# Optimization experiments

Hardware: AMD Instinct MI355X
Metric: run time of the kernel (lower is better)

The kernel has to match this reference:

```python
import jax, jax.numpy as jnp
import numpy as np

B, N, D, H = 8, 1024, 512, 8
DH = D // H  # one_head_dim = 64


def setup_inputs() -> dict:
    key = jax.random.key(0)
    ks = jax.random.split(key, 7)
    s = 0.02
    return {
        "x": jax.random.normal(ks[0], (B, N, D), dtype=jnp.float32),
        "bias": jax.random.normal(ks[1], (B, N, N, H), dtype=jnp.float32),
        "Wq": jax.random.normal(ks[2], (D, D), dtype=jnp.float32) * s,
        "Wk": jax.random.normal(ks[3], (D, D), dtype=jnp.float32) * s,
        "Wv": jax.random.normal(ks[4], (D, D), dtype=jnp.float32) * s,
        "Wm": jax.random.normal(ks[5], (D, D), dtype=jnp.float32) * s,
        "bm": jnp.zeros((D,), dtype=jnp.float32),
    }


def reference(x, bias, Wq, Wk, Wv, Wm, bm):
    # Linear layers (torch Linear: y = x @ W.T); dropout is identity at eval.
    scale = DH ** -0.5
    q = (x @ Wq.T).reshape(B, N, H, DH).transpose(0, 2, 1, 3) * scale  # [B,H,N,DH]
    k = (x @ Wk.T).reshape(B, N, H, DH).transpose(0, 2, 1, 3)
    v = (x @ Wv.T).reshape(B, N, H, DH).transpose(0, 2, 1, 3)
    # scores + additive pairwise bias (bias permuted [B,N,N,H] -> [B,H,N,N])
    scores = jnp.einsum("bhnd,bhmd->bhnm", q, k) + bias.transpose(0, 3, 1, 2)
    attn = jax.nn.softmax(scores, axis=-1)
    out = jnp.einsum("bhnm,bhmd->bhnd", attn, v)  # [B,H,N,DH]
    out = out.transpose(0, 2, 1, 3).reshape(B, N, D)
    return out @ Wm.T + bm
```

## Files before the change

kernel.cpp:

```cpp
#include <hip/hip_runtime.h>
#include <hip/hip_bf16.h>

typedef __bf16 bf16x8 __attribute__((ext_vector_type(8)));
typedef __bf16 bf16x4 __attribute__((ext_vector_type(4)));
typedef float  f32x4  __attribute__((ext_vector_type(4)));

#define MFMA16(a, b, c) __builtin_amdgcn_mfma_f32_16x16x32_bf16((a), (b), (c), 0, 0, 0)

typedef const __attribute__((address_space(1))) unsigned int* gas_t;
typedef __attribute__((address_space(3))) unsigned int* las_t;
__device__ __forceinline__ void dma16(const __bf16* g, __bf16* l) {
    __builtin_amdgcn_global_load_lds((gas_t)g, (las_t)l, 16, 0, 0);
}


__global__ __launch_bounds__(256) void gemm_qkv(
    const float* __restrict__ x,
    const float* __restrict__ Wq, const float* __restrict__ Wk,
    const float* __restrict__ Wv,
    __bf16* __restrict__ qo, __bf16* __restrict__ ko, __bf16* __restrict__ vto)
{
    __shared__ __bf16 As[64][40];
    __shared__ __bf16 Bs[3][64][40];
    const int tid  = threadIdx.x;
    const int lane = tid & 63;
    const int wid  = tid >> 6;
    const int g    = lane >> 4, l16 = lane & 15;
    const int wr   = wid >> 1,  wc  = wid & 1;
    const int r0   = blockIdx.x * 64;
    const int c0   = blockIdx.y * 64;
    const float* Ws[3] = { Wq, Wk, Wv };

    const int sr  = tid >> 3;
    const int scq = tid & 7;

    f32x4 acc[3][2][2] = {};

    for (int k0 = 0; k0 < 512; k0 += 32) {
        __syncthreads();
#pragma unroll
        for (int j = 0; j < 2; ++j) {
            const int r = sr + 32 * j;
            float4 av = *reinterpret_cast<const float4*>(x + (size_t)(r0 + r) * 512 + k0 + scq * 4);
            bf16x4 ap = { (__bf16)av.x, (__bf16)av.y, (__bf16)av.z, (__bf16)av.w };
            *reinterpret_cast<bf16x4*>(&As[r][scq * 4]) = ap;
#pragma unroll
            for (int widx = 0; widx < 3; ++widx) {
                float4 bv = *reinterpret_cast<const float4*>(Ws[widx] + (size_t)(c0 + r) * 512 + k0 + scq * 4);
                bf16x4 bp = { (__bf16)bv.x, (__bf16)bv.y, (__bf16)bv.z, (__bf16)bv.w };
                *reinterpret_cast<bf16x4*>(&Bs[widx][r][scq * 4]) = bp;
            }
        }
        __syncthreads();
        bf16x8 af[2];
#pragma unroll
        for (int rt = 0; rt < 2; ++rt)
            af[rt] = *reinterpret_cast<const bf16x8*>(&As[wr * 32 + rt * 16 + l16][g * 8]);
#pragma unroll
        for (int widx = 0; widx < 3; ++widx) {
            bf16x8 bfr[2];
#pragma unroll
            for (int ct = 0; ct < 2; ++ct)
                bfr[ct] = *reinterpret_cast<const bf16x8*>(&Bs[widx][wc * 32 + ct * 16 + l16][g * 8]);
#pragma unroll
            for (int rt = 0; rt < 2; ++rt)
#pragma unroll
                for (int ct = 0; ct < 2; ++ct)
                    acc[widx][rt][ct] = MFMA16(af[rt], bfr[ct], acc[widx][rt][ct]);
        }
    }

#pragma unroll
    for (int widx = 0; widx < 2; ++widx) {
        __bf16* dst = (widx == 0) ? qo : ko;
        const float scale = (widx == 0) ? 0.125f : 1.0f;
#pragma unroll
        for (int rt = 0; rt < 2; ++rt)
#pragma unroll
            for (int ct = 0; ct < 2; ++ct)
#pragma unroll
                for (int reg = 0; reg < 4; ++reg) {
                    int r = r0 + wr * 32 + rt * 16 + 4 * g + reg;
                    int c = c0 + wc * 32 + ct * 16 + l16;
                    float val = acc[widx][rt][ct][reg] * scale;
                    int b = r >> 10, n = r & 1023, h = c >> 6, dh = c & 63;
                    dst[(((size_t)b * 8 + h) * 1024 + n) * 64 + dh] = (__bf16)val;
                }
    }
#pragma unroll
    for (int rt = 0; rt < 2; ++rt)
#pragma unroll
        for (int ct = 0; ct < 2; ++ct) {
            int r = r0 + wr * 32 + rt * 16 + 4 * g;
            int c = c0 + wc * 32 + ct * 16 + l16;
            int b = r >> 10, n = r & 1023, h = c >> 6, dh = c & 63;
            bf16x4 pv = { (__bf16)acc[2][rt][ct][0], (__bf16)acc[2][rt][ct][1],
                          (__bf16)acc[2][rt][ct][2], (__bf16)acc[2][rt][ct][3] };
            size_t addr = (((size_t)(b * 8 + h) * 32 + (n >> 5)) * 64 + dh) * 32 + (n & 31);
            *reinterpret_cast<bf16x4*>(vto + addr) = pv;
        }
}

__global__ __launch_bounds__(512, 2) void attn_v12(
    const __bf16* __restrict__ qw, const __bf16* __restrict__ kw,
    const __bf16* __restrict__ vtw, const float* __restrict__ bias,
    __bf16* __restrict__ ow)
{
    __shared__ __align__(16) __bf16 Ks[8][32][64];
    __shared__ __align__(16) __bf16 Vs[8][64][32];
    __shared__ __align__(16) __bf16 bsm[2][8][32][36];
    __shared__ __bf16 psm[8][32][40];
    const int tid  = threadIdx.x;
    const int w    = tid >> 6;
    const int lane = tid & 63;
    const int g    = lane >> 4, l16 = lane & 15;
    const int b    = blockIdx.x;
    const int n0   = blockIdx.y * 32;
    const size_t bhs = (size_t)b * 8 + w;

    const __bf16* kbase  = kw  + bhs * 1024 * 64;
    const __bf16* vbase  = vtw + bhs * 32 * 2048;
    const float*  bias_b = bias + ((size_t)(b * 1024 + n0)) * 8192;

    const int snr = tid >> 4;
    const int sf  = tid & 15;

    const int k_row  = lane >> 3;
    const int k_csrc = (lane & 7) ^ (k_row & 7);
    const int v_dh   = lane >> 2;
    const int v_csrc = (lane & 3) ^ ((lane >> 3) & 3);
    const int v_rsw  = (l16 >> 1) & 3;

    bf16x8 qf[2][2];
#pragma unroll
    for (int rf = 0; rf < 2; ++rf)
#pragma unroll
        for (int kc = 0; kc < 2; ++kc)
            qf[rf][kc] = *reinterpret_cast<const bf16x8*>(
                qw + (bhs * 1024 + n0 + rf * 16 + l16) * 64 + kc * 32 + g * 8);

    f32x4 o[2][4] = {};
    float lrun[2][4] = {};

    f32x4 bpA[4], bpB[4];

#define LOAD_BIAS(dst, tt)                                                     \
    {                                                                          \
        const int m0_ = (tt) * 32;                                             \
        _Pragma("unroll")                                                      \
        for (int c = 0; c < 4; ++c)                                            \
            dst[c] = __builtin_nontemporal_load(reinterpret_cast<const f32x4*>(\
                bias_b + (size_t)snr * 8192 + m0_ * 8 + (sf + 16 * c) * 4));   \
    }

#define WRITE_BIAS(buf, src)                                                   \
    {                                                                          \
        _Pragma("unroll")                                                      \
        for (int c = 0; c < 4; ++c) {                                          \
            const int f4 = sf + 16 * c;                                        \
            const int mm = f4 >> 1, h0 = (f4 & 1) * 4;                         \
            bsm[buf][h0 + 0][mm][snr] = (__bf16)src[c].x;                      \
            bsm[buf][h0 + 1][mm][snr] = (__bf16)src[c].y;                      \
            bsm[buf][h0 + 2][mm][snr] = (__bf16)src[c].z;                      \
            bsm[buf][h0 + 3][mm][snr] = (__bf16)src[c].w;                      \
        }                                                                      \
    }

#define DMA_KV(tt)                                                             \
    {                                                                          \
        const int m0_ = (tt) * 32;                                             \
        _Pragma("unroll")                                                      \
        for (int i = 0; i < 4; ++i)                                            \
            dma16(kbase + (size_t)(m0_ + i * 8 + k_row) * 64 + k_csrc * 8,     \
                  &Ks[w][i * 8][0]);                                           \
        const __bf16* vblk = vbase + (size_t)(tt) * 2048;                      \
        _Pragma("unroll")                                                      \
        for (int i = 0; i < 4; ++i)                                            \
            dma16(vblk + (size_t)(i * 16 + v_dh) * 32 + v_csrc * 8,            \
                  &Vs[w][i * 16][0]);                                          \
    }

    LOAD_BIAS(bpA, 0)
    DMA_KV(0)
    WRITE_BIAS(0, bpA)
    LOAD_BIAS(bpA, 1)
    LOAD_BIAS(bpB, 2)
    asm volatile("s_waitcnt vmcnt(8)");
    __builtin_amdgcn_sched_barrier(0);
    asm volatile("s_waitcnt lgkmcnt(0)");
    __builtin_amdgcn_s_barrier();
    __builtin_amdgcn_sched_barrier(0);

#define ATTN_STEP(t, BUF, bpX)                                                 \
    {                                                                          \
        bf16x8 kf[2][2], vf[4];                                                \
        _Pragma("unroll")                                                      \
        for (int ct = 0; ct < 2; ++ct)                                         \
            _Pragma("unroll")                                                  \
            for (int kc = 0; kc < 2; ++kc) {                                   \
                const int mrow = ct * 16 + l16;                                \
                kf[ct][kc] = *reinterpret_cast<const bf16x8*>(                 \
                    &Ks[w][mrow][(((kc * 4 + g) ^ (l16 & 7)) * 8)]);           \
            }                                                                  \
        _Pragma("unroll")                                                      \
        for (int oc = 0; oc < 4; ++oc)                                         \
            vf[oc] = *reinterpret_cast<const bf16x8*>(                         \
                &Vs[w][oc * 16 + l16][(g ^ v_rsw) * 8]);                       \
        bf16x4 bb[2][2];                                                       \
        _Pragma("unroll")                                                      \
        for (int rf = 0; rf < 2; ++rf)                                         \
            _Pragma("unroll")                                                  \
            for (int ct = 0; ct < 2; ++ct)                                     \
                bb[rf][ct] = *reinterpret_cast<const bf16x4*>(                 \
                    &bsm[BUF][w][ct * 16 + l16][rf * 16 + 4 * g]);             \
                     \
        asm volatile("s_waitcnt lgkmcnt(0)");                                  \
        __builtin_amdgcn_sched_barrier(0);                                     \
        DMA_KV((t) + 1 < 32 ? (t) + 1 : 31)                                    \
        f32x4 s[2][2] = {};                                                    \
        _Pragma("unroll")                                                      \
        for (int rf = 0; rf < 2; ++rf)                                         \
            _Pragma("unroll")                                                  \
            for (int ct = 0; ct < 2; ++ct) {                                   \
                s[rf][ct] = MFMA16(qf[rf][0], kf[ct][0], s[rf][ct]);           \
                s[rf][ct] = MFMA16(qf[rf][1], kf[ct][1], s[rf][ct]);           \
            }                                                                  \
        _Pragma("unroll")                                                      \
        for (int rf = 0; rf < 2; ++rf)                                         \
            _Pragma("unroll")                                                  \
            for (int reg = 0; reg < 4; ++reg) {                                \
                const int nr = rf * 16 + 4 * g + reg;                          \
                float p0 = __expf(s[rf][0][reg] + (float)bb[rf][0][reg] - 16.0f); \
                float p1 = __expf(s[rf][1][reg] + (float)bb[rf][1][reg] - 16.0f); \
                lrun[rf][reg] += p0 + p1;                                      \
                psm[w][nr][l16]      = (__bf16)p0;                             \
                psm[w][nr][16 + l16] = (__bf16)p1;                             \
            }                                                                  \
        bf16x8 pf[2];                                                          \
        _Pragma("unroll")                                                      \
        for (int rf = 0; rf < 2; ++rf)                                         \
            pf[rf] = *reinterpret_cast<const bf16x8*>(&psm[w][rf * 16 + l16][g * 8]); \
        _Pragma("unroll")                                                      \
        for (int rf = 0; rf < 2; ++rf)                                         \
            _Pragma("unroll")                                                  \
            for (int oc = 0; oc < 4; ++oc)                                     \
                o[rf][oc] = MFMA16(pf[rf], vf[oc], o[rf][oc]);                 \
                        \
        WRITE_BIAS((BUF) ^ 1, bpX)                                             \
        LOAD_BIAS(bpX, (t) + 3 < 32 ? (t) + 3 : 31)                            \
                    \
        asm volatile("s_waitcnt vmcnt(4)");                                    \
        __builtin_amdgcn_sched_barrier(0);                                     \
        asm volatile("s_waitcnt lgkmcnt(0)");                                  \
        __builtin_amdgcn_s_barrier();                                          \
        __builtin_amdgcn_sched_barrier(0);                                     \
    }

    for (int t = 0; t < 32; t += 2) {
        ATTN_STEP(t,     0, bpA)
        ATTN_STEP(t + 1, 1, bpB)
    }
#undef ATTN_STEP
#undef LOAD_BIAS
#undef WRITE_BIAS
#undef DMA_KV

#pragma unroll
    for (int rf = 0; rf < 2; ++rf)
#pragma unroll
        for (int reg = 0; reg < 4; ++reg) {
            float l = lrun[rf][reg];
            l += __shfl_xor(l, 1);
            l += __shfl_xor(l, 2);
            l += __shfl_xor(l, 4);
            l += __shfl_xor(l, 8);
            lrun[rf][reg] = l;
        }

#pragma unroll
    for (int rf = 0; rf < 2; ++rf)
#pragma unroll
        for (int oc = 0; oc < 4; ++oc)
#pragma unroll
            for (int reg = 0; reg < 4; ++reg) {
                int n  = n0 + rf * 16 + 4 * g + reg;
                int dh = oc * 16 + l16;
                float val = o[rf][oc][reg] / lrun[rf][reg];
                ow[((size_t)b * 1024 + n) * 512 + w * 64 + dh] = (__bf16)val;
            }
}

__global__ __launch_bounds__(256) void gemm_out(
    const __bf16* __restrict__ a, const float* __restrict__ Wm,
    const float* __restrict__ bm, float* __restrict__ out)
{
    __shared__ __bf16 As[64][40];
    __shared__ __bf16 Bs[64][40];
    const int tid  = threadIdx.x;
    const int lane = tid & 63;
    const int wid  = tid >> 6;
    const int g    = lane >> 4, l16 = lane & 15;
    const int wr   = wid >> 1,  wc  = wid & 1;
    const int r0   = blockIdx.x * 64;
    const int c0   = blockIdx.y * 64;

    const int sra = tid >> 2, sca = tid & 3;
    const int srb = tid >> 3, scb = tid & 7;

    f32x4 acc[2][2] = {};
    for (int k0 = 0; k0 < 512; k0 += 32) {
        __syncthreads();
        {
            bf16x8 av = *reinterpret_cast<const bf16x8*>(a + (size_t)(r0 + sra) * 512 + k0 + sca * 8);
            *reinterpret_cast<bf16x8*>(&As[sra][sca * 8]) = av;
#pragma unroll
            for (int j = 0; j < 2; ++j) {
                int r = srb + 32 * j;
                float4 bv = *reinterpret_cast<const float4*>(Wm + (size_t)(c0 + r) * 512 + k0 + scb * 4);
                bf16x4 bp = { (__bf16)bv.x, (__bf16)bv.y, (__bf16)bv.z, (__bf16)bv.w };
                *reinterpret_cast<bf16x4*>(&Bs[r][scb * 4]) = bp;
            }
        }
        __syncthreads();
        bf16x8 af[2], bfr[2];
#pragma unroll
        for (int rt = 0; rt < 2; ++rt)
            af[rt] = *reinterpret_cast<const bf16x8*>(&As[wr * 32 + rt * 16 + l16][g * 8]);
#pragma unroll
        for (int ct = 0; ct < 2; ++ct)
            bfr[ct] = *reinterpret_cast<const bf16x8*>(&Bs[wc * 32 + ct * 16 + l16][g * 8]);
#pragma unroll
        for (int rt = 0; rt < 2; ++rt)
#pragma unroll
            for (int ct = 0; ct < 2; ++ct)
                acc[rt][ct] = MFMA16(af[rt], bfr[ct], acc[rt][ct]);
    }

#pragma unroll
    for (int rt = 0; rt < 2; ++rt)
#pragma unroll
        for (int ct = 0; ct < 2; ++ct)
#pragma unroll
            for (int reg = 0; reg < 4; ++reg) {
                int r = r0 + wr * 32 + rt * 16 + 4 * g + reg;
                int c = c0 + wc * 32 + ct * 16 + l16;
                out[(size_t)r * 512 + c] = acc[rt][ct][reg] + bm[c];
            }
}

extern "C" void kernel_launch(void* const* d_in, const int* in_sizes, int n_in,
                              void* d_out, int out_size, void* d_ws, size_t ws_size,
                              hipStream_t stream)
{
    const float* x    = (const float*)d_in[0];
    const float* bias = (const float*)d_in[1];
    const float* Wq   = (const float*)d_in[2];
    const float* Wk   = (const float*)d_in[3];
    const float* Wv   = (const float*)d_in[4];
    const float* Wm   = (const float*)d_in[5];
    const float* bm   = (const float*)d_in[6];
    float* out = (float*)d_out;

    const size_t SEG = (size_t)8 * 8 * 1024 * 64;
    __bf16* qw  = (__bf16*)d_ws;
    __bf16* kw  = qw + SEG;
    __bf16* vtw = kw + SEG;
    __bf16* ow  = vtw + SEG;

    gemm_qkv<<<dim3(128, 8), 256, 0, stream>>>(x, Wq, Wk, Wv, qw, kw, vtw);
    attn_v12<<<dim3(8, 32), 512, 0, stream>>>(qw, kw, vtw, bias, ow);
    gemm_out<<<dim3(128, 8), 256, 0, stream>>>(ow, Wm, bm, out);
}
```

Baseline: 130.6 us.

## Use 128x128 tiles in QKV and output GEMMs, split QKV by weight

Both projection GEMMs move from 64x64 to 128x128 output tiles, with each wave computing a 4x4 grid of MFMA tiles. The QKV kernel no longer computes all three weights per block; the grid's y dimension now selects the weight matrix. The goal is more reuse of each staged tile and fewer redundant loads of x and the weights. The cost is fewer blocks (768 and 256), which may underfill the CUs, and higher per-thread register use.

```diff
diff --git a/kernel.cpp b/kernel.cpp
--- a/kernel.cpp
+++ b/kernel.cpp
@@ -20,85 +20,76 @@
     const float* __restrict__ Wv,
     __bf16* __restrict__ qo, __bf16* __restrict__ ko, __bf16* __restrict__ vto)
 {
-    __shared__ __bf16 As[64][40];
-    __shared__ __bf16 Bs[3][64][40];
+    __shared__ __bf16 As[128][40];
+    __shared__ __bf16 Bs[128][40];
     const int tid  = threadIdx.x;
     const int lane = tid & 63;
     const int wid  = tid >> 6;
     const int g    = lane >> 4, l16 = lane & 15;
     const int wr   = wid >> 1,  wc  = wid & 1;
-    const int r0   = blockIdx.x * 64;
-    const int c0   = blockIdx.y * 64;
-    const float* Ws[3] = { Wq, Wk, Wv };
-
-    const int sr  = tid >> 3;
-    const int scq = tid & 7;
-
-    f32x4 acc[3][2][2] = {};
+    const int r0   = blockIdx.x * 128;
+    const int widx = blockIdx.y >> 2;
+    const int c0   = (blockIdx.y & 3) * 128;
+    const float* W = (widx == 0) ? Wq : (widx == 1 ? Wk : Wv);
+
+    f32x4 acc[4][4] = {};
 
     for (int k0 = 0; k0 < 512; k0 += 32) {
         __syncthreads();
 #pragma unroll
-        for (int j = 0; j < 2; ++j) {
-            const int r = sr + 32 * j;
-            float4 av = *reinterpret_cast<const float4*>(x + (size_t)(r0 + r) * 512 + k0 + scq * 4);
+        for (int j = 0; j < 4; ++j) {
+            const int idx = tid + 256 * j;
+            const int r = idx >> 3, c4 = (idx & 7) * 4;
+            f32x4 av = *reinterpret_cast<const f32x4*>(x + (size_t)(r0 + r) * 512 + k0 + c4);
+            f32x4 bv = *reinterpret_cast<const f32x4*>(W + (size_t)(c0 + r) * 512 + k0 + c4);
             bf16x4 ap = { (__bf16)av.x, (__bf16)av.y, (__bf16)av.z, (__bf16)av.w };
-            *reinterpret_cast<bf16x4*>(&As[r][scq * 4]) = ap;
-#pragma unroll
-            for (int widx = 0; widx < 3; ++widx) {
-                float4 bv = *reinterpret_cast<const float4*>(Ws[widx] + (size_t)(c0 + r) * 512 + k0 + scq * 4);
-                bf16x4 bp = { (__bf16)bv.x, (__bf16)bv.y, (__bf16)bv.z, (__bf16)bv.w };
-                *reinterpret_cast<bf16x4*>(&Bs[widx][r][scq * 4]) = bp;
+            bf16x4 bp = { (__bf16)bv.x, (__bf16)bv.y, (__bf16)bv.z, (__bf16)bv.w };
+            *reinterpret_cast<bf16x4*>(&As[r][c4]) = ap;
+            *reinterpret_cast<bf16x4*>(&Bs[r][c4]) = bp;
+        }
+        __syncthreads();
+        bf16x8 af[4], bfr[4];
+#pragma unroll
+        for (int i = 0; i < 4; ++i) {
+            af[i]  = *reinterpret_cast<const bf16x8*>(&As[wr * 64 + i * 16 + l16][g * 8]);
+            bfr[i] = *reinterpret_cast<const bf16x8*>(&Bs[wc * 64 + i * 16 + l16][g * 8]);
+        }
+#pragma unroll
+        for (int i = 0; i < 4; ++i)
+#pragma unroll
+            for (int j = 0; j < 4; ++j)
+                acc[i][j] = MFMA16(af[i], bfr[j], acc[i][j]);
+    }
+
+    if (widx == 2) {
+#pragma unroll
+        for (int rt = 0; rt < 4; ++rt)
+#pragma unroll
+            for (int ct = 0; ct < 4; ++ct) {
+                int r = r0 + wr * 64 + rt * 16 + 4 * g;
+                int c = c0 + wc * 64 + ct * 16 + l16;
+                int b = r >> 10, n = r & 1023, h = c >> 6, dh = c & 63;
+                bf16x4 pv = { (__bf16)acc[rt][ct][0], (__bf16)acc[rt][ct][1],
+                              (__bf16)acc[rt][ct][2], (__bf16)acc[rt][ct][3] };
+                size_t addr = (((size_t)(b * 8 + h) * 32 + (n >> 5)) * 64 + dh) * 32 + (n & 31);
+                *reinterpret_cast<bf16x4*>(vto + addr) = pv;
             }
-        }
-        __syncthreads();
-        bf16x8 af[2];
-#pragma unroll
-        for (int rt = 0; rt < 2; ++rt)
-            af[rt] = *reinterpret_cast<const bf16x8*>(&As[wr * 32 + rt * 16 + l16][g * 8]);
-#pragma unroll
-        for (int widx = 0; widx < 3; ++widx) {
-            bf16x8 bfr[2];
-#pragma unroll
-            for (int ct = 0; ct < 2; ++ct)
-                bfr[ct] = *reinterpret_cast<const bf16x8*>(&Bs[widx][wc * 32 + ct * 16 + l16][g * 8]);
-#pragma unroll
-            for (int rt = 0; rt < 2; ++rt)
-#pragma unroll
-                for (int ct = 0; ct < 2; ++ct)
-                    acc[widx][rt][ct] = MFMA16(af[rt], bfr[ct], acc[widx][rt][ct]);
-        }
-    }
-
-#pragma unroll
-    for (int widx = 0; widx < 2; ++widx) {
+    } else {
         __bf16* dst = (widx == 0) ? qo : ko;
         const float scale = (widx == 0) ? 0.125f : 1.0f;
 #pragma unroll
-        for (int rt = 0; rt < 2; ++rt)
-#pragma unroll
-            for (int ct = 0; ct < 2; ++ct)
+        for (int rt = 0; rt < 4; ++rt)
+#pragma unroll
+            for (int ct = 0; ct < 4; ++ct)
 #pragma unroll
                 for (int reg = 0; reg < 4; ++reg) {
-                    int r = r0 + wr * 32 + rt * 16 + 4 * g + reg;
-                    int c = c0 + wc * 32 + ct * 16 + l16;
-                    float val = acc[widx][rt][ct][reg] * scale;
+                    int r = r0 + wr * 64 + rt * 16 + 4 * g + reg;
+                    int c = c0 + wc * 64 + ct * 16 + l16;
+                    float val = acc[rt][ct][reg] * scale;
                     int b = r >> 10, n = r & 1023, h = c >> 6, dh = c & 63;
                     dst[(((size_t)b * 8 + h) * 1024 + n) * 64 + dh] = (__bf16)val;
                 }
     }
-#pragma unroll
-    for (int rt = 0; rt < 2; ++rt)
-#pragma unroll
-        for (int ct = 0; ct < 2; ++ct) {
-            int r = r0 + wr * 32 + rt * 16 + 4 * g;
-            int c = c0 + wc * 32 + ct * 16 + l16;
-            int b = r >> 10, n = r & 1023, h = c >> 6, dh = c & 63;
-            bf16x4 pv = { (__bf16)acc[2][rt][ct][0], (__bf16)acc[2][rt][ct][1],
-                          (__bf16)acc[2][rt][ct][2], (__bf16)acc[2][rt][ct][3] };
-            size_t addr = (((size_t)(b * 8 + h) * 32 + (n >> 5)) * 64 + dh) * 32 + (n & 31);
-            *reinterpret_cast<bf16x4*>(vto + addr) = pv;
-        }
 }
 
 __global__ __launch_bounds__(512, 2) void attn_v12(
@@ -294,56 +285,57 @@
     const __bf16* __restrict__ a, const float* __restrict__ Wm,
     const float* __restrict__ bm, float* __restrict__ out)
 {
-    __shared__ __bf16 As[64][40];
-    __shared__ __bf16 Bs[64][40];
+    __shared__ __bf16 As[128][40];
+    __shared__ __bf16 Bs[128][40];
     const int tid  = threadIdx.x;
     const int lane = tid & 63;
     const int wid  = tid >> 6;
     const int g    = lane >> 4, l16 = lane & 15;
     const int wr   = wid >> 1,  wc  = wid & 1;
-    const int r0   = blockIdx.x * 64;
-    const int c0   = blockIdx.y * 64;
-
-    const int sra = tid >> 2, sca = tid & 3;
-    const int srb = tid >> 3, scb = tid & 7;
-
-    f32x4 acc[2][2] = {};
+    const int r0   = blockIdx.x * 128;
+    const int c0   = blockIdx.y * 128;
+
+    f32x4 acc[4][4] = {};
+
     for (int k0 = 0; k0 < 512; k0 += 32) {
         __syncthreads();
-        {
-            bf16x8 av = *reinterpret_cast<const bf16x8*>(a + (size_t)(r0 + sra) * 512 + k0 + sca * 8);
-            *reinterpret_cast<bf16x8*>(&As[sra][sca * 8]) = av;
-#pragma unroll
-            for (int j = 0; j < 2; ++j) {
-                int r = srb + 32 * j;
-                float4 bv = *reinterpret_cast<const float4*>(Wm + (size_t)(c0 + r) * 512 + k0 + scb * 4);
-                bf16x4 bp = { (__bf16)bv.x, (__bf16)bv.y, (__bf16)bv.z, (__bf16)bv.w };
-                *reinterpret_cast<bf16x4*>(&Bs[r][scb * 4]) = bp;
-            }
+#pragma unroll
+        for (int j = 0; j < 2; ++j) {
+            const int idx = tid + 256 * j;
+            const int r = idx >> 2, c8 = (idx & 3) * 8;
+            bf16x8 av = *reinterpret_cast<const bf16x8*>(a + (size_t)(r0 + r) * 512 + k0 + c8);
+            *reinterpret_cast<bf16x8*>(&As[r][c8]) = av;
+        }
+#pragma unroll
+        for (int j = 0; j < 4; ++j) {
+            const int idx = tid + 256 * j;
+            const int r = idx >> 3, c4 = (idx & 7) * 4;
+            f32x4 bv = *reinterpret_cast<const f32x4*>(Wm + (size_t)(c0 + r) * 512 + k0 + c4);
+            bf16x4 bp = { (__bf16)bv.x, (__bf16)bv.y, (__bf16)bv.z, (__bf16)bv.w };
+            *reinterpret_cast<bf16x4*>(&Bs[r][c4]) = bp;
         }
         __syncthreads();
-        bf16x8 af[2], bfr[2];
-#pragma unroll
-        for (int rt = 0; rt < 2; ++rt)
-            af[rt] = *reinterpret_cast<const bf16x8*>(&As[wr * 32 + rt * 16 + l16][g * 8]);
-#pragma unroll
-        for (int ct = 0; ct < 2; ++ct)
-            bfr[ct] = *reinterpret_cast<const bf16x8*>(&Bs[wc * 32 + ct * 16 + l16][g * 8]);
-#pragma unroll
-        for (int rt = 0; rt < 2; ++rt)
-#pragma unroll
-            for (int ct = 0; ct < 2; ++ct)
-                acc[rt][ct] = MFMA16(af[rt], bfr[ct], acc[rt][ct]);
-    }
-
-#pragma unroll
-    for (int rt = 0; rt < 2; ++rt)
-#pragma unroll
-        for (int ct = 0; ct < 2; ++ct)
+        bf16x8 af[4], bfr[4];
+#pragma unroll
+        for (int i = 0; i < 4; ++i) {
+            af[i]  = *reinterpret_cast<const bf16x8*>(&As[wr * 64 + i * 16 + l16][g * 8]);
+            bfr[i] = *reinterpret_cast<const bf16x8*>(&Bs[wc * 64 + i * 16 + l16][g * 8]);
+        }
+#pragma unroll
+        for (int i = 0; i < 4; ++i)
+#pragma unroll
+            for (int j = 0; j < 4; ++j)
+                acc[i][j] = MFMA16(af[i], bfr[j], acc[i][j]);
+    }
+
+#pragma unroll
+    for (int rt = 0; rt < 4; ++rt)
+#pragma unroll
+        for (int ct = 0; ct < 4; ++ct)
 #pragma unroll
             for (int reg = 0; reg < 4; ++reg) {
-                int r = r0 + wr * 32 + rt * 16 + 4 * g + reg;
-                int c = c0 + wc * 32 + ct * 16 + l16;
+                int r = r0 + wr * 64 + rt * 16 + 4 * g + reg;
+                int c = c0 + wc * 64 + ct * 16 + l16;
                 out[(size_t)r * 512 + c] = acc[rt][ct][reg] + bm[c];
             }
 }
@@ -367,7 +359,7 @@
     __bf16* vtw = kw + SEG;
     __bf16* ow  = vtw + SEG;
 
-    gemm_qkv<<<dim3(128, 8), 256, 0, stream>>>(x, Wq, Wk, Wv, qw, kw, vtw);
+    gemm_qkv<<<dim3(64, 12), 256, 0, stream>>>(x, Wq, Wk, Wv, qw, kw, vtw);
     attn_v12<<<dim3(8, 32), 512, 0, stream>>>(qw, kw, vtw, bias, ow);
-    gemm_out<<<dim3(128, 8), 256, 0, stream>>>(ow, Wm, bm, out);
-}
+    gemm_out<<<dim3(64, 4), 256, 0, stream>>>(ow, Wm, bm, out);
+}
```

New measurement: 124.4 us. 4.8% less time.
